# Performance work log

Hardware: AMD Instinct MI355X
Metric: run time of the kernel (lower is better)

The kernel has to match this reference:

```python
import jax, jax.numpy as jnp
import numpy as np

B, S, N, F, H = 8, 12, 4096, 4, 64  # batch, seq_len, num_nodes, input_dim, hidden_dim


def setup_inputs() -> dict:
    key = jax.random.key(0)
    ks = jax.random.split(key, 16)
    sc = 0.05
    adj = jax.random.uniform(ks[0], (N, N), jnp.float32) * (2.0 / N)  # ~row-normalized Laplacian
    return {
        "X": jax.random.normal(ks[1], (B, S, N, F), jnp.float32),
        "adj": adj,
        "struc_emb": jax.random.normal(ks[2], (N, H), jnp.float32),
        "W1": jax.random.normal(ks[3], (H + F, 3 * H), jnp.float32) * sc,
        "b1": jnp.ones((3 * H,), jnp.float32),  # bias=1.0 init in graph_conv1
        "W2": jax.random.normal(ks[4], (H + F, H), jnp.float32) * sc,
        "b2": jnp.zeros((H,), jnp.float32),
        "W_ih": jax.random.normal(ks[5], (4 * H, H), jnp.float32) * sc,
        "W_hh": jax.random.normal(ks[6], (4 * H, H), jnp.float32) * sc,
        "b_ih": jnp.zeros((4 * H,), jnp.float32),
        "b_hh": jnp.zeros((4 * H,), jnp.float32),
        "D1": jax.random.normal(ks[7], (H, H // 2), jnp.float32) * sc,
        "bd1": jnp.zeros((H // 2,), jnp.float32),
        "D2": jax.random.normal(ks[8], (H // 2, 1), jnp.float32) * sc,
        "bd2": jnp.zeros((1,), jnp.float32),
    }


def _graph_conv(adj, x_t, h_flat, W, b, out_dim):
    # x_t: [B,N,F]; h_flat: [B, N*H]
    h = h_flat.reshape(B, N, H)
    cat = jnp.concatenate([x_t, h], axis=-1)            # [B,N,F+H]
    a = jnp.einsum('mn,bnf->bmf', adj, cat)             # laplacian diffusion
    out = a @ W + b                                     # [B,N,out_dim]
    return out.reshape(B, N * out_dim)


def reference(X, adj, struc_emb, W1, b1, W2, b2, W_ih, W_hh, b_ih, b_hh, D1, bd1, D2, bd2):
    # ---- encoder: TGTCCellLSTM unrolled over time (cell_state never updated, as in source) ----
    h0 = jnp.broadcast_to(struc_emb.reshape(1, N * H), (B, N * H))
    c0 = h0  # cell returns old cell_state, so it stays the struc_emb forever (faithful)

    def enc_step(h, x_t):
        g = jax.nn.sigmoid(_graph_conv(adj, x_t, h, W1, b1, 3 * H))   # [B, N*3H]
        f, i, o = jnp.split(g, 3, axis=1)                             # flat chunk, as in torch code
        conv = _graph_conv(adj, x_t, h, W2, b2, H)                    # [B, N*H]
        c = f * c0 + i * jnp.tanh(conv)
        h_new = o * jnp.tanh(c)
        return h_new, None

    h_last, _ = jax.lax.scan(enc_step, h0, jnp.swapaxes(X, 0, 1))  # scan over S
    z = h_last.reshape(B, N, H)

    # ---- decoder: 1-layer LSTM fed the same z at every step, then 2-layer MLP to scalar ----
    x_dec = z.reshape(B * N, H)
    x_gates = x_dec @ W_ih.T + b_ih + b_hh  # input contribution constant across steps

    def dec_step(carry, _):
        h, c = carry
        gates = x_gates + h @ W_hh.T
        i, f, g, o = jnp.split(gates, 4, axis=1)  # torch LSTM gate order
        c = jax.nn.sigmoid(f) * c + jax.nn.sigmoid(i) * jnp.tanh(g)
        h = jax.nn.sigmoid(o) * jnp.tanh(c)
        return (h, c), h

    zeros = jnp.zeros((B * N, H), X.dtype)
    _, hs = jax.lax.scan(dec_step, (zeros, zeros), None, length=S)  # [S, B*N, H]
    hs = jnp.swapaxes(hs, 0, 1)                                      # [B*N, S, H]
    d = jax.nn.relu(hs @ D1 + bd1) @ D2 + bd2                        # [B*N, S, 1]
    recon = d.reshape(B, S, N)  # flat reshape from (B*N, S), matching torch reshape semantics
    return (z, recon)
```

## Files before the change

kernel.cpp:

```cpp
#include <hip/hip_runtime.h>
#include <cstdint>
#include <cstddef>


typedef unsigned short u16;
typedef short s8v __attribute__((ext_vector_type(8)));
typedef unsigned short h8v __attribute__((ext_vector_type(8)));
typedef float f4v __attribute__((ext_vector_type(4)));
typedef int   i4v __attribute__((ext_vector_type(4)));

__device__ __forceinline__ u16 f2bf(float x){
  union { float f; uint32_t u; } v; v.f = x;
  uint32_t r = v.u + 0x7FFFu + ((v.u >> 16) & 1u);
  return (u16)(r >> 16);
}
__device__ __forceinline__ float bf2f(u16 x){
  union { uint32_t u; float f; } v; v.u = ((uint32_t)x) << 16; return v.f;
}
__device__ __forceinline__ float frcp(float x){ return __builtin_amdgcn_rcpf(x); }
__device__ __forceinline__ float fsig(float x){ return frcp(1.0f + __expf(-x)); }
__device__ __forceinline__ float ftanh(float x){ return 1.0f - 2.0f * frcp(1.0f + __expf(2.0f * x)); }
__device__ __forceinline__ int8_t f2i8(float x){
  int v = (int)rintf(x);
  v = v > 127 ? 127 : (v < -127 ? -127 : v);
  return (int8_t)v;
}

typedef const __attribute__((address_space(1))) unsigned int* gp_t;
typedef __attribute__((address_space(3))) unsigned int* lp_t;
__device__ __forceinline__ void glds16(const void* g, void* l){
  __builtin_amdgcn_global_load_lds((gp_t)g, (lp_t)l, 16, 0, 0);
}

__global__ __launch_bounds__(256)
void gemm_s1_i8(const int8_t* __restrict__ A, const int8_t* __restrict__ Bt,
                u16* __restrict__ Cpart, int Ncols, int ksl, float cscale)
{
  __shared__ int8_t As[2 * 128 * 128];
  __shared__ int8_t Bs[2 * 128 * 128];
  const int t  = threadIdx.x;
  const int l  = t & 63;
  const int w  = t >> 6;
  const int wm = (w >> 1) * 64;
  const int wc = (w & 1) * 64;
  const int mb = blockIdx.x * 128;
  const int nb = blockIdx.y * 128;
  const int k0 = blockIdx.z * ksl;

  i4v acc[4][4];
  #pragma unroll
  for (int i = 0; i < 4; ++i)
    #pragma unroll
    for (int j = 0; j < 4; ++j) acc[i][j] = (i4v)0;

  const int srow = t >> 3;
  const int gsw  = ((t & 7) ^ (srow & 7)) * 16;
  const int8_t* ab = A  + (size_t)(mb + srow) * 4096 + k0 + gsw;
  const int8_t* bb = Bt + (size_t)(nb + srow) * 4096 + k0 + gsw;

  const int rA = l & 15;
  const int lsw = l & 7;

  #pragma unroll
  for (int j = 0; j < 4; ++j) {
    glds16(ab + (size_t)(32 * j) * 4096, As + j * 4096 + t * 16);
    glds16(bb + (size_t)(32 * j) * 4096, Bs + j * 4096 + t * 16);
  }

  for (int kk = 0; kk < ksl; kk += 128) {
    const int cur = (kk >> 7) & 1;
    __syncthreads();
    if (kk + 128 < ksl) {
      const int nxt = cur ^ 1;
      #pragma unroll
      for (int j = 0; j < 4; ++j) {
        glds16(ab + (size_t)(32 * j) * 4096 + kk + 128, As + nxt * 16384 + j * 4096 + t * 16);
        glds16(bb + (size_t)(32 * j) * 4096 + kk + 128, Bs + nxt * 16384 + j * 4096 + t * 16);
      }
    }
    const int bofs = cur * 16384;
    #pragma unroll
    for (int sub = 0; sub < 2; ++sub) {
      const int kpos = ((sub * 4 + (l >> 4)) ^ lsw) * 16;
      i4v af[4], bf[4];
      #pragma unroll
      for (int mt = 0; mt < 4; ++mt)
        af[mt] = *(const i4v*)&As[bofs + (wm + mt * 16 + rA) * 128 + kpos];
      #pragma unroll
      for (int nt = 0; nt < 4; ++nt)
        bf[nt] = *(const i4v*)&Bs[bofs + (wc + nt * 16 + rA) * 128 + kpos];
      #pragma unroll
      for (int mt = 0; mt < 4; ++mt)
        #pragma unroll
        for (int nt = 0; nt < 4; ++nt)
          acc[mt][nt] = __builtin_amdgcn_mfma_i32_16x16x64_i8(af[mt], bf[nt], acc[mt][nt], 0, 0, 0);
    }
  }

  u16* Cs = Cpart + (size_t)blockIdx.z * 4096 * Ncols;
  const int colo = l & 15;
  const int rowo = (l >> 4) * 4;
  #pragma unroll
  for (int mt = 0; mt < 4; ++mt)
    #pragma unroll
    for (int nt = 0; nt < 4; ++nt)
      #pragma unroll
      for (int r = 0; r < 4; ++r) {
        int gr = mb + wm + mt * 16 + rowo + r;
        int gc = nb + wc + nt * 16 + colo;
        Cs[(size_t)gr * Ncols + gc] = f2bf((float)acc[mt][nt][r] * cscale);
      }
}

__global__ __launch_bounds__(256)
void reduceN(const u16* __restrict__ P, u16* __restrict__ O, size_t SL)
{
  size_t i = ((size_t)blockIdx.x * 256 + threadIdx.x) * 8;
  if (i >= SL) return;
  float s[8] = {0,0,0,0,0,0,0,0};
  #pragma unroll
  for (int z = 0; z < 4; ++z) {
    uint4 v = *(const uint4*)(P + z * SL + i);
    uint32_t wd[4] = {v.x, v.y, v.z, v.w};
    #pragma unroll
    for (int q = 0; q < 4; ++q) {
      union { uint32_t u; float f; } lo, hi;
      lo.u = wd[q] << 16; hi.u = wd[q] & 0xFFFF0000u;
      s[2*q] += lo.f; s[2*q+1] += hi.f;
    }
  }
  uint4 o; uint32_t* ow = (uint32_t*)&o;
  #pragma unroll
  for (int q = 0; q < 4; ++q)
    ow[q] = (uint32_t)f2bf(s[2*q]) | ((uint32_t)f2bf(s[2*q+1]) << 16);
  *(uint4*)(O + i) = o;
}

__global__ __launch_bounds__(256)
void gemm_s2(const u16* __restrict__ AH, const u16* __restrict__ AXb,
             const u16* __restrict__ WT, const float* __restrict__ b1v,
             const float* __restrict__ b2v, u16* __restrict__ G, int tstep)
{
  __shared__ u16 As[64*104];
  __shared__ u16 Bs[256*104];
  const int t = threadIdx.x;
  const int l = t & 63, w = t >> 6;
  const int wm = (w >> 1) * 32, wc0 = (w & 1) * 32;
  const int mb = blockIdx.x * 64;
  const size_t SL = 32768ull * 64;

  #pragma unroll
  for (int pass = 0; pass < 2; ++pass) {
    int idx = t + pass * 256;
    int row = idx >> 3, oct = idx & 7;
    size_t base = (size_t)(mb + row) * 64 + oct * 8;
    float s[8] = {0,0,0,0,0,0,0,0};
    #pragma unroll
    for (int z = 0; z < 4; ++z) {
      uint4 v = *(const uint4*)(AH + z * SL + base);
      uint32_t wd[4] = {v.x, v.y, v.z, v.w};
      #pragma unroll
      for (int q = 0; q < 4; ++q) {
        union { uint32_t u; float f; } lo, hi;
        lo.u = wd[q] << 16; hi.u = wd[q] & 0xFFFF0000u;
        s[2*q] += lo.f; s[2*q+1] += hi.f;
      }
    }
    uint4 o; uint32_t* ow = (uint32_t*)&o;
    #pragma unroll
    for (int q = 0; q < 4; ++q)
      ow[q] = (uint32_t)f2bf(s[2*q]) | ((uint32_t)f2bf(s[2*q+1]) << 16);
    *(uint4*)&As[row * 104 + oct * 8] = o;
  }
  {
    int row = t >> 2, q = t & 3;
    uint4 o = {0, 0, 0, 0};
    if (q == 0) {
      int r = mb + row, n = r >> 3, b = r & 7;
      const uint32_t* src = (const uint32_t*)(AXb + (size_t)n * 384 + tstep * 32 + b * 4);
      o.x = src[0]; o.y = src[1];
    }
    *(uint4*)&As[row * 104 + 64 + q * 8] = o;
  }
  #pragma unroll
  for (int pass = 0; pass < 12; ++pass) {
    int idx = t + pass * 256;
    int row = idx / 12, seg = idx - row * 12;
    *(uint4*)&Bs[row * 104 + seg * 8] = *(const uint4*)(WT + (size_t)row * 96 + seg * 8);
  }
  __syncthreads();

  const int rA = l & 15, kg = (l >> 4) * 8;
  s8v af[3][2];
  #pragma unroll
  for (int kc = 0; kc < 3; ++kc)
    #pragma unroll
    for (int mt = 0; mt < 2; ++mt)
      af[kc][mt] = *(const s8v*)&As[(wm + mt * 16 + rA) * 104 + kc * 32 + kg];

  const int colo = l & 15, rowo = (l >> 4) * 4;
  #pragma unroll
  for (int nb4 = 0; nb4 < 4; ++nb4) {
    const int wc = nb4 * 64 + wc0;
    f4v acc[2][2];
    #pragma unroll
    for (int i = 0; i < 2; ++i)
      #pragma unroll
      for (int j = 0; j < 2; ++j) acc[i][j] = (f4v)0.0f;
    #pragma unroll
    for (int kc = 0; kc < 3; ++kc) {
      s8v bf[2];
      #pragma unroll
      for (int nt = 0; nt < 2; ++nt)
        bf[nt] = *(const s8v*)&Bs[(wc + nt * 16 + rA) * 104 + kc * 32 + kg];
      #pragma unroll
      for (int mt = 0; mt < 2; ++mt)
        #pragma unroll
        for (int nt = 0; nt < 2; ++nt)
          acc[mt][nt] = __builtin_amdgcn_mfma_f32_16x16x32_bf16(af[kc][mt], bf[nt], acc[mt][nt], 0, 0, 0);
    }

    #pragma unroll
    for (int mt = 0; mt < 2; ++mt)
      #pragma unroll
      for (int nt = 0; nt < 2; ++nt) {
        int gc = wc + nt * 16 + colo;
        float bb = (gc < 192) ? b1v[gc] : b2v[gc - 192];
        #pragma unroll
        for (int r = 0; r < 4; ++r) {
          int gr = mb + wm + mt * 16 + rowo + r;
          int np = gr >> 3, b = gr & 7;
          float v = acc[mt][nt][r] + bb;
          size_t addr;
          u16 val;
          if (gc < 192) {
            int p = np * 192 + gc;
            int role = p >> 18;
            int k = p & 262143;
            addr = ((size_t)(role * 8 + b) << 18) + k;
            val = f2bf(fsig(v));
          } else {
            int k = np * 64 + (gc - 192);
            addr = ((size_t)(24 + b) << 18) + k;
            val = f2bf(ftanh(v));
          }
          G[addr] = val;
        }
      }
  }
}

__global__ void conv_adj_i8(const float* __restrict__ adj, int8_t* __restrict__ out){
  size_t i = ((size_t)blockIdx.x * 256 + threadIdx.x) * 4;
  float4 v = *(const float4*)(adj + i);
  const float s = 127.0f * 2048.0f;
  char4 o;
  o.x = f2i8(v.x * s); o.y = f2i8(v.y * s); o.z = f2i8(v.z * s); o.w = f2i8(v.w * s);
  *(char4*)(out + i) = o;
}

__global__ void build_w(const float* __restrict__ W1, const float* __restrict__ W2,
                        const float* __restrict__ Wih, const float* __restrict__ Whh,
                        const float* __restrict__ D1,
                        u16* __restrict__ WT, u16* __restrict__ WihB,
                        u16* __restrict__ WhhB, u16* __restrict__ D1t){
  int gid = blockIdx.x * 256 + threadIdx.x;
  if (gid < 24576) {
    int j = gid / 96, ch = gid - j * 96;
    float v = 0.0f;
    int rr = (ch < 64) ? (ch + 4) : (ch < 68 ? ch - 64 : -1);
    if (rr >= 0) v = (j < 192) ? W1[(size_t)rr * 192 + j] : W2[(size_t)rr * 64 + (j - 192)];
    WT[gid] = f2bf(v);
  } else if (gid < 40960) {
    int q = gid - 24576; WihB[q] = f2bf(Wih[q]);
  } else if (gid < 57344) {
    int q = gid - 40960; WhhB[q] = f2bf(Whh[q]);
  } else if (gid < 59392) {
    int q = gid - 57344;
    int j = q >> 6, hh = q & 63;
    D1t[q] = f2bf(D1[(size_t)hh * 32 + j]);
  }
}

__global__ void init_pb(const float* __restrict__ struc, int8_t* __restrict__ PB){
  int gid = blockIdx.x * 256 + threadIdx.x;
  int n = gid & 4095;
  int r = gid >> 12;
  int hh = r & 63;
  PB[(size_t)r * 4096 + n] = f2i8(struc[(size_t)n * 64 + hh] * 25.4f);
}

__global__ void pack_xall(const float* __restrict__ X, int8_t* __restrict__ Xp){
  int gid = blockIdx.x * 256 + threadIdx.x;
  int n = gid & 4095;
  int col = gid >> 12;
  int ts = col >> 5, r = col & 31, b = r >> 2, f = r & 3;
  Xp[(size_t)col * 4096 + n] = f2i8(X[(((size_t)(b * 12 + ts)) * 4096 + n) * 4 + f] * 25.4f);
}

__global__ __launch_bounds__(256)
void enc_update(const u16* __restrict__ G, const float* __restrict__ struc,
                int8_t* __restrict__ PB, float* __restrict__ zout,
                u16* __restrict__ zbf, int last)
{
  __shared__ uint8_t hx[64 * 40];
  const int t = threadIdx.x;
  const int b = blockIdx.x >> 7;
  const int n0 = (blockIdx.x & 127) * 32;
  const int k8 = n0 * 64 + t * 8;
  const int nloc = t >> 3;
  const int hh0 = (t & 7) * 8;

  h8v f8 = *(const h8v*)&G[((size_t)(     b) << 18) + k8];
  h8v i8_ = *(const h8v*)&G[((size_t)( 8 + b) << 18) + k8];
  h8v o8 = *(const h8v*)&G[((size_t)(16 + b) << 18) + k8];
  h8v c8 = *(const h8v*)&G[((size_t)(24 + b) << 18) + k8];
  float4 s0 = *(const float4*)&struc[k8];
  float4 s1 = *(const float4*)&struc[k8 + 4];
  float sv[8] = {s0.x, s0.y, s0.z, s0.w, s1.x, s1.y, s1.z, s1.w};

  float hv[8];
  #pragma unroll
  for (int j = 0; j < 8; ++j) {
    float c = bf2f(f8[j]) * sv[j] + bf2f(i8_[j]) * bf2f(c8[j]);
    hv[j] = bf2f(o8[j]) * ftanh(c);
    hx[(hh0 + j) * 40 + nloc] = (uint8_t)f2i8(hv[j] * 127.0f);
  }
  if (last) {
    float4 z0 = {hv[0], hv[1], hv[2], hv[3]};
    float4 z1 = {hv[4], hv[5], hv[6], hv[7]};
    *(float4*)&zout[((size_t)b << 18) + k8] = z0;
    *(float4*)&zout[((size_t)b << 18) + k8 + 4] = z1;
    h8v zb;
    #pragma unroll
    for (int j = 0; j < 8; ++j) zb[j] = f2bf(hv[j]);
    *(h8v*)&zbf[((size_t)b << 18) + k8] = zb;
  }
  __syncthreads();
  {
    int row = t >> 2, seg = t & 3;
    uint2 v = *(const uint2*)&hx[row * 40 + seg * 8];
    *(uint2*)&PB[(size_t)(b * 64 + row) * 4096 + n0 + seg * 8] = v;
  }
}

__global__ __launch_bounds__(256)
void dec_fused(const u16* __restrict__ zbf, const u16* __restrict__ WihB,
               const u16* __restrict__ WhhB,
               const float* __restrict__ bih, const float* __restrict__ bhh,
               const u16* __restrict__ D1t, const float* __restrict__ bd1,
               const float* __restrict__ D2, const float* __restrict__ bd2,
               float* __restrict__ recon)
{
  __shared__ u16 whl[256 * 72];
  __shared__ u16 hl[64 * 72];
  const int t = threadIdx.x;
  const int l = t & 63;
  const int w = t >> 6;
  const int r0 = blockIdx.x * 64;
  const int rA = l & 15;
  const int kg = (l >> 4) * 8;

  for (int c = t; c < 2048; c += 256) {
    int j = c >> 3, k8 = (c & 7) * 8;
    *(uint4*)&whl[j * 72 + k8] = *(const uint4*)&WhhB[j * 64 + k8];
  }

  f4v xg[16];
  {
    s8v a0 = *(const s8v*)&zbf[(size_t)(r0 + w * 16 + rA) * 64 + kg];
    s8v a1 = *(const s8v*)&zbf[(size_t)(r0 + w * 16 + rA) * 64 + 32 + kg];
    #pragma unroll
    for (int nt = 0; nt < 16; ++nt) {
      s8v b0 = *(const s8v*)&WihB[(nt * 16 + rA) * 64 + kg];
      s8v b1 = *(const s8v*)&WihB[(nt * 16 + rA) * 64 + 32 + kg];
      f4v a = (f4v)0.0f;
      a = __builtin_amdgcn_mfma_f32_16x16x32_bf16(a0, b0, a, 0, 0, 0);
      a = __builtin_amdgcn_mfma_f32_16x16x32_bf16(a1, b1, a, 0, 0, 0);
      float bb = bih[nt * 16 + rA] + bhh[nt * 16 + rA];
      #pragma unroll
      for (int r = 0; r < 4; ++r) xg[nt][r] = a[r] + bb;
    }
  }
  s8v d1f[4];
  #pragma unroll
  for (int nt = 0; nt < 2; ++nt)
    #pragma unroll
    for (int kc = 0; kc < 2; ++kc)
      d1f[nt * 2 + kc] = *(const s8v*)&D1t[(nt * 16 + rA) * 64 + kc * 32 + kg];
  const float bd1x = bd1[rA], bd1y = bd1[16 + rA];
  const float d2x = D2[rA], d2y = D2[16 + rA];
  const float bd2v = bd2[0];

  float cst[16];
  #pragma unroll
  for (int q = 0; q < 16; ++q) cst[q] = 0.0f;
  s8v ha0 = (s8v)0, ha1 = (s8v)0;
  __syncthreads();

  for (int s = 0; s < 12; ++s) {
    f4v acc[16];
    #pragma unroll
    for (int nt = 0; nt < 16; ++nt) acc[nt] = xg[nt];
    if (s > 0) {
      #pragma unroll
      for (int nt = 0; nt < 16; ++nt) {
        s8v b0 = *(const s8v*)&whl[(nt * 16 + rA) * 72 + kg];
        s8v b1 = *(const s8v*)&whl[(nt * 16 + rA) * 72 + 32 + kg];
        acc[nt] = __builtin_amdgcn_mfma_f32_16x16x32_bf16(ha0, b0, acc[nt], 0, 0, 0);
        acc[nt] = __builtin_amdgcn_mfma_f32_16x16x32_bf16(ha1, b1, acc[nt], 0, 0, 0);
      }
    }
    #pragma unroll
    for (int q = 0; q < 4; ++q)
      #pragma unroll
      for (int r = 0; r < 4; ++r) {
        float i_ = fsig (acc[q     ][r]);
        float f_ = fsig (acc[q + 4 ][r]);
        float g_ = ftanh(acc[q + 8 ][r]);
        float o_ = fsig (acc[q + 12][r]);
        float cc = f_ * cst[q * 4 + r] + i_ * g_;
        cst[q * 4 + r] = cc;
        float hv = o_ * ftanh(cc);
        hl[(w * 16 + (l >> 4) * 4 + r) * 72 + q * 16 + rA] = f2bf(hv);
      }
    ha0 = *(const s8v*)&hl[(w * 16 + rA) * 72 + kg];
    ha1 = *(const s8v*)&hl[(w * 16 + rA) * 72 + 32 + kg];
    f4v m0 = (f4v)0.0f, m1 = (f4v)0.0f;
    m0 = __builtin_amdgcn_mfma_f32_16x16x32_bf16(ha0, d1f[0], m0, 0, 0, 0);
    m0 = __builtin_amdgcn_mfma_f32_16x16x32_bf16(ha1, d1f[1], m0, 0, 0, 0);
    m1 = __builtin_amdgcn_mfma_f32_16x16x32_bf16(ha0, d1f[2], m1, 0, 0, 0);
    m1 = __builtin_amdgcn_mfma_f32_16x16x32_bf16(ha1, d1f[3], m1, 0, 0, 0);
    f4v p;
    #pragma unroll
    for (int r = 0; r < 4; ++r)
      p[r] = fmaxf(m0[r] + bd1x, 0.0f) * d2x + fmaxf(m1[r] + bd1y, 0.0f) * d2y;
    #pragma unroll
    for (int mask = 1; mask < 16; mask <<= 1)
      #pragma unroll
      for (int r = 0; r < 4; ++r) p[r] += __shfl_xor(p[r], mask);
    if (rA < 4)
      recon[(size_t)(r0 + w * 16 + (l >> 4) * 4 + rA) * 12 + s] = p[rA] + bd2v;
  }
}

extern "C" void kernel_launch(void* const* d_in, const int* in_sizes, int n_in,
                              void* d_out, int out_size, void* d_ws, size_t ws_size,
                              hipStream_t stream)
{
  (void)in_sizes; (void)n_in; (void)out_size; (void)ws_size;
  const float* X     = (const float*)d_in[0];
  const float* adj   = (const float*)d_in[1];
  const float* struc = (const float*)d_in[2];
  const float* W1    = (const float*)d_in[3];
  const float* b1    = (const float*)d_in[4];
  const float* W2    = (const float*)d_in[5];
  const float* b2    = (const float*)d_in[6];
  const float* Wih   = (const float*)d_in[7];
  const float* Whh   = (const float*)d_in[8];
  const float* bih   = (const float*)d_in[9];
  const float* bhh   = (const float*)d_in[10];
  const float* D1    = (const float*)d_in[11];
  const float* bd1   = (const float*)d_in[12];
  const float* D2    = (const float*)d_in[13];
  const float* bd2   = (const float*)d_in[14];

  char* ws = (char*)d_ws;
  size_t off = 0;
  auto alloc = [&](size_t bytes){ void* p = ws + off; off += (bytes + 255) & ~(size_t)255; return p; };
  int8_t* adj_i8 = (int8_t*)alloc(4096ull * 4096);
  int8_t* PB     = (int8_t*)alloc(512ull * 4096);
  int8_t* Xp     = (int8_t*)alloc(384ull * 4096);
  u16*   AXb    = (u16*)  alloc(4096ull * 384 * 2);
  u16*   Cpart  = (u16*)  alloc(4ull * 4096 * 512 * 2);
  u16*   G      = (u16*)  alloc(4ull * 8 * 262144 * 2);
  u16*   zbf    = (u16*)  alloc(32768ull * 64 * 2);
  u16*   WT     = (u16*)  alloc(256ull * 96 * 2);
  u16*   WihB   = (u16*)  alloc(256ull * 64 * 2);
  u16*   WhhB   = (u16*)  alloc(256ull * 64 * 2);
  u16*   D1t    = (u16*)  alloc(32ull * 64 * 2);

  float* zout  = (float*)d_out;
  float* recon = (float*)d_out + 2097152;

  const float cs5 = (float)(2.0 / 4096.0 * 5.0 / (127.0 * 127.0));
  const float cs1 = (float)(2.0 / 4096.0 * 1.0 / (127.0 * 127.0));

  conv_adj_i8<<<16384, 256, 0, stream>>>(adj, adj_i8);
  build_w    <<<  232, 256, 0, stream>>>(W1, W2, Wih, Whh, D1, WT, WihB, WhhB, D1t);
  init_pb    <<< 8192, 256, 0, stream>>>(struc, PB);
  pack_xall  <<< 6144, 256, 0, stream>>>(X, Xp);
  gemm_s1_i8 <<<dim3(32, 3, 4), 256, 0, stream>>>(adj_i8, Xp, Cpart, 384, 1024, cs5);
  reduceN    <<<  768, 256, 0, stream>>>(Cpart, AXb, 4096ull * 384);

  for (int t = 0; t < 12; ++t) {
    gemm_s1_i8<<<dim3(32, 4, 4), 256, 0, stream>>>(adj_i8, PB, Cpart, 512, 1024,
                                                   t == 0 ? cs5 : cs1);
    gemm_s2<<<512, 256, 0, stream>>>(Cpart, AXb, WT, b1, b2, G, t);
    enc_update<<<1024, 256, 0, stream>>>(G, struc, PB, zout, zbf, t == 11);
  }

  dec_fused<<<512, 256, 0, stream>>>(zbf, WihB, WhhB, bih, bhh,
                                     D1t, bd1, D2, bd2, recon);
}
```

Before: 570.1 us.

## Split decoder LSTM gate columns across two waves per row tile

The fused decoder now runs 512 threads per block, and each pair of waves shares one 16-row tile, with each wave computing half of the hidden columns for all four gates. This halves per-wave accumulator and state registers and doubles the number of waves available to hide MFMA and transcendental latency. The cost is two block-wide barriers per time step, because the h tile is now produced by two waves before either can read it back, and half of the waves sit idle during the MLP head.

```diff
diff --git a/kernel.cpp b/kernel.cpp
--- a/kernel.cpp
+++ b/kernel.cpp
@@ -344,7 +344,7 @@
   }
 }
 
-__global__ __launch_bounds__(256)
+__global__ __launch_bounds__(512, 4)
 void dec_fused(const u16* __restrict__ zbf, const u16* __restrict__ WihB,
                const u16* __restrict__ WhhB,
                const float* __restrict__ bih, const float* __restrict__ bhh,
@@ -357,21 +357,24 @@
   const int t = threadIdx.x;
   const int l = t & 63;
   const int w = t >> 6;
+  const int wg = w >> 1;
+  const int half = w & 1;
   const int r0 = blockIdx.x * 64;
   const int rA = l & 15;
   const int kg = (l >> 4) * 8;
 
-  for (int c = t; c < 2048; c += 256) {
+  for (int c = t; c < 2048; c += 512) {
     int j = c >> 3, k8 = (c & 7) * 8;
     *(uint4*)&whl[j * 72 + k8] = *(const uint4*)&WhhB[j * 64 + k8];
   }
 
-  f4v xg[16];
+  f4v xg[8];
   {
-    s8v a0 = *(const s8v*)&zbf[(size_t)(r0 + w * 16 + rA) * 64 + kg];
-    s8v a1 = *(const s8v*)&zbf[(size_t)(r0 + w * 16 + rA) * 64 + 32 + kg];
-    #pragma unroll
-    for (int nt = 0; nt < 16; ++nt) {
+    s8v a0 = *(const s8v*)&zbf[(size_t)(r0 + wg * 16 + rA) * 64 + kg];
+    s8v a1 = *(const s8v*)&zbf[(size_t)(r0 + wg * 16 + rA) * 64 + 32 + kg];
+    #pragma unroll
+    for (int j = 0; j < 8; ++j) {
+      int nt = (j >> 1) * 4 + half * 2 + (j & 1);
       s8v b0 = *(const s8v*)&WihB[(nt * 16 + rA) * 64 + kg];
       s8v b1 = *(const s8v*)&WihB[(nt * 16 + rA) * 64 + 32 + kg];
       f4v a = (f4v)0.0f;
@@ -379,68 +382,75 @@
       a = __builtin_amdgcn_mfma_f32_16x16x32_bf16(a1, b1, a, 0, 0, 0);
       float bb = bih[nt * 16 + rA] + bhh[nt * 16 + rA];
       #pragma unroll
-      for (int r = 0; r < 4; ++r) xg[nt][r] = a[r] + bb;
+      for (int r = 0; r < 4; ++r) xg[j][r] = a[r] + bb;
     }
   }
   s8v d1f[4];
   #pragma unroll
-  for (int nt = 0; nt < 2; ++nt)
+  for (int nt2 = 0; nt2 < 2; ++nt2)
     #pragma unroll
     for (int kc = 0; kc < 2; ++kc)
-      d1f[nt * 2 + kc] = *(const s8v*)&D1t[(nt * 16 + rA) * 64 + kc * 32 + kg];
+      d1f[nt2 * 2 + kc] = *(const s8v*)&D1t[(nt2 * 16 + rA) * 64 + kc * 32 + kg];
   const float bd1x = bd1[rA], bd1y = bd1[16 + rA];
   const float d2x = D2[rA], d2y = D2[16 + rA];
   const float bd2v = bd2[0];
 
-  float cst[16];
-  #pragma unroll
-  for (int q = 0; q < 16; ++q) cst[q] = 0.0f;
+  float cst[8];
+  #pragma unroll
+  for (int q = 0; q < 8; ++q) cst[q] = 0.0f;
   s8v ha0 = (s8v)0, ha1 = (s8v)0;
   __syncthreads();
 
   for (int s = 0; s < 12; ++s) {
-    f4v acc[16];
-    #pragma unroll
-    for (int nt = 0; nt < 16; ++nt) acc[nt] = xg[nt];
+    f4v acc[8];
+    #pragma unroll
+    for (int j = 0; j < 8; ++j) acc[j] = xg[j];
     if (s > 0) {
       #pragma unroll
-      for (int nt = 0; nt < 16; ++nt) {
+      for (int j = 0; j < 8; ++j) {
+        int nt = (j >> 1) * 4 + half * 2 + (j & 1);
         s8v b0 = *(const s8v*)&whl[(nt * 16 + rA) * 72 + kg];
         s8v b1 = *(const s8v*)&whl[(nt * 16 + rA) * 72 + 32 + kg];
-        acc[nt] = __builtin_amdgcn_mfma_f32_16x16x32_bf16(ha0, b0, acc[nt], 0, 0, 0);
-        acc[nt] = __builtin_amdgcn_mfma_f32_16x16x32_bf16(ha1, b1, acc[nt], 0, 0, 0);
+        acc[j] = __builtin_amdgcn_mfma_f32_16x16x32_bf16(ha0, b0, acc[j], 0, 0, 0);
+        acc[j] = __builtin_amdgcn_mfma_f32_16x16x32_bf16(ha1, b1, acc[j], 0, 0, 0);
       }
     }
-    #pragma unroll
-    for (int q = 0; q < 4; ++q)
+    __syncthreads();
+    #pragma unroll
+    for (int ql = 0; ql < 2; ++ql) {
+      int q = half * 2 + ql;
       #pragma unroll
       for (int r = 0; r < 4; ++r) {
-        float i_ = fsig (acc[q     ][r]);
-        float f_ = fsig (acc[q + 4 ][r]);
-        float g_ = ftanh(acc[q + 8 ][r]);
-        float o_ = fsig (acc[q + 12][r]);
-        float cc = f_ * cst[q * 4 + r] + i_ * g_;
-        cst[q * 4 + r] = cc;
+        float i_ = fsig (acc[0 + ql][r]);
+        float f_ = fsig (acc[2 + ql][r]);
+        float g_ = ftanh(acc[4 + ql][r]);
+        float o_ = fsig (acc[6 + ql][r]);
+        float cc = f_ * cst[ql * 4 + r] + i_ * g_;
+        cst[ql * 4 + r] = cc;
         float hv = o_ * ftanh(cc);
-        hl[(w * 16 + (l >> 4) * 4 + r) * 72 + q * 16 + rA] = f2bf(hv);
+        hl[(wg * 16 + (l >> 4) * 4 + r) * 72 + q * 16 + rA] = f2bf(hv);
       }
-    ha0 = *(const s8v*)&hl[(w * 16 + rA) * 72 + kg];
-    ha1 = *(const s8v*)&hl[(w * 16 + rA) * 72 + 32 + kg];
-    f4v m0 = (f4v)0.0f, m1 = (f4v)0.0f;
-    m0 = __builtin_amdgcn_mfma_f32_16x16x32_bf16(ha0, d1f[0], m0, 0, 0, 0);
-    m0 = __builtin_amdgcn_mfma_f32_16x16x32_bf16(ha1, d1f[1], m0, 0, 0, 0);
-    m1 = __builtin_amdgcn_mfma_f32_16x16x32_bf16(ha0, d1f[2], m1, 0, 0, 0);
-    m1 = __builtin_amdgcn_mfma_f32_16x16x32_bf16(ha1, d1f[3], m1, 0, 0, 0);
-    f4v p;
-    #pragma unroll
-    for (int r = 0; r < 4; ++r)
-      p[r] = fmaxf(m0[r] + bd1x, 0.0f) * d2x + fmaxf(m1[r] + bd1y, 0.0f) * d2y;
-    #pragma unroll
-    for (int mask = 1; mask < 16; mask <<= 1)
-      #pragma unroll
-      for (int r = 0; r < 4; ++r) p[r] += __shfl_xor(p[r], mask);
-    if (rA < 4)
-      recon[(size_t)(r0 + w * 16 + (l >> 4) * 4 + rA) * 12 + s] = p[rA] + bd2v;
+    }
+    __syncthreads();
+    ha0 = *(const s8v*)&hl[(wg * 16 + rA) * 72 + kg];
+    ha1 = *(const s8v*)&hl[(wg * 16 + rA) * 72 + 32 + kg];
+    if (half == 0) {
+      f4v m0 = (f4v)0.0f, m1 = (f4v)0.0f;
+      m0 = __builtin_amdgcn_mfma_f32_16x16x32_bf16(ha0, d1f[0], m0, 0, 0, 0);
+      m0 = __builtin_amdgcn_mfma_f32_16x16x32_bf16(ha1, d1f[1], m0, 0, 0, 0);
+      m1 = __builtin_amdgcn_mfma_f32_16x16x32_bf16(ha0, d1f[2], m1, 0, 0, 0);
+      m1 = __builtin_amdgcn_mfma_f32_16x16x32_bf16(ha1, d1f[3], m1, 0, 0, 0);
+      f4v p;
+      #pragma unroll
+      for (int r = 0; r < 4; ++r)
+        p[r] = fmaxf(m0[r] + bd1x, 0.0f) * d2x + fmaxf(m1[r] + bd1y, 0.0f) * d2y;
+      #pragma unroll
+      for (int mask = 1; mask < 16; mask <<= 1)
+        #pragma unroll
+        for (int r = 0; r < 4; ++r) p[r] += __shfl_xor(p[r], mask);
+      if (rA < 4)
+        recon[(size_t)(r0 + wg * 16 + (l >> 4) * 4 + rA) * 12 + s] = p[rA] + bd2v;
+    }
   }
 }
 
@@ -500,6 +510,6 @@
     enc_update<<<1024, 256, 0, stream>>>(G, struc, PB, zout, zbf, t == 11);
   }
 
-  dec_fused<<<512, 256, 0, stream>>>(zbf, WihB, WhhB, bih, bhh,
+  dec_fused<<<512, 512, 0, stream>>>(zbf, WihB, WhhB, bih, bhh,
                                      D1t, bd1, D2, bd2, recon);
 }
```

Measured after the change: 562.3 us. No clear change (-1.4%).
